# Performance work log

Hardware: AMD Instinct MI355X
Metric: run time of the kernel (lower is better)

Reference implementation:

```python
import jax, jax.numpy as jnp
import numpy as np

DIM, BIN = 128, 16
LN_EPS = 1e-5


def setup_inputs() -> dict:
    key = jax.random.key(0)
    ks = jax.random.split(key, 16)
    B, Ld, Lc, O = 4096, 50, 50, 64
    D_VOCAB, C_VOCAB = 100000, 1000
    inp = {
        "discrete_index": jax.random.randint(ks[0], (B, Ld), 0, D_VOCAB, dtype=jnp.int32),
        "discrete_mask": jax.random.randint(ks[1], (B, Ld), 0, 2, dtype=jnp.int32),
        "continue_value": jax.random.normal(ks[2], (B, Lc), dtype=jnp.float32),
        "continue_index": jax.random.randint(ks[3], (B, Lc), 0, C_VOCAB, dtype=jnp.int32),
        "continue_mask": jax.random.randint(ks[4], (B, Lc), 0, 2, dtype=jnp.int32),
        # learned parameters (last row = padding idx, zeroed like torch padding_idx init semantics)
        "disc_emb": jax.random.normal(ks[5], (D_VOCAB + 1, DIM), dtype=jnp.float32).at[D_VOCAB].set(0.0),
        "v_emb": jax.random.normal(ks[6], (C_VOCAB + 1, BIN), dtype=jnp.float32).at[C_VOCAB].set(0.0),
        "b1_emb": jax.random.normal(ks[7], (C_VOCAB + 1, BIN), dtype=jnp.float32).at[C_VOCAB].set(0.0),
        "w_emb": jax.random.normal(ks[8], (C_VOCAB + 1, DIM * BIN), dtype=jnp.float32).at[C_VOCAB].set(0.0),
        "b2_emb": jax.random.normal(ks[9], (C_VOCAB + 1, DIM), dtype=jnp.float32).at[C_VOCAB].set(0.0),
        "ln_gamma": jnp.ones((BIN,), dtype=jnp.float32),
        "ln_beta": jnp.zeros((BIN,), dtype=jnp.float32),
        "transform_matrix": jax.random.normal(ks[10], (O, Ld + Lc), dtype=jnp.float32),
    }
    return inp


def reference(discrete_index, discrete_mask, continue_value, continue_index, continue_mask,
              disc_emb, v_emb, b1_emb, w_emb, b2_emb, ln_gamma, ln_beta, transform_matrix):
    B, Lc = continue_index.shape
    # embedding gathers
    discrete_part = disc_emb[discrete_index]            # [B, Ld, D]
    v = v_emb[continue_index]                           # [B, Lc, BIN]
    b1 = b1_emb[continue_index]                         # [B, Lc, BIN]
    w = w_emb[continue_index].reshape(B, Lc, BIN, DIM)  # [B, Lc, BIN, D]
    b2 = b2_emb[continue_index]                         # [B, Lc, D]
    # per-token mini-MLP: LayerNorm(bin) + ReLU + bmm with per-token weight
    h = continue_value[..., None] * v + b1              # [B, Lc, BIN]
    mu = jnp.mean(h, axis=-1, keepdims=True)
    var = jnp.mean((h - mu) ** 2, axis=-1, keepdims=True)
    hn = (h - mu) * jax.lax.rsqrt(var + LN_EPS) * ln_gamma + ln_beta
    a = jax.nn.relu(hn)
    continuous_part = jnp.einsum('blk,blkd->bld', a, w) + b2  # [B, Lc, D]
    parts = jnp.concatenate([discrete_part, continuous_part], axis=1)  # [B, L, D]
    out = jnp.einsum('ol,bld->bod', transform_matrix, parts)           # [B, O, D]
    # mask (no-grad path in original)
    mvec = jnp.concatenate([1 - discrete_mask, 1 - continue_mask], axis=1).astype(jnp.float32)  # [B, L]
    full_mask = (1.0 - jnp.sign(jnp.einsum('ol,bl->bo', transform_matrix, mvec))).astype(jnp.int32)  # [B, O]
    return out, full_mask
```

## Files before the change

### kernel.cpp

```cpp
#include <hip/hip_runtime.h>
#include <hip/hip_bf16.h>

#define NB 4096
#define LD_ 50
#define LC_ 50
#define LTOT 100
#define DIM 128
#define BIN 16
#define NO 64
#define KPAD 128
#define LP 136
#define LN_EPS 1e-5f

#define DISC_ELEMS 12800128
#define DISC_VEC8  1600016
#define DISC_BLKS  6251
#define W_VEC8     256256
#define W_BLKS     1001
#define T_BLKS     32
#define CONV_BLKS  (DISC_BLKS + W_BLKS + T_BLKS)

typedef __attribute__((ext_vector_type(8))) short bf16x8;
typedef __attribute__((ext_vector_type(4))) float f32x4;

__device__ __forceinline__ unsigned f2bf(float f) {
    return (unsigned)__builtin_bit_cast(unsigned short, __float2bfloat16(f));
}
__device__ __forceinline__ float bf2f(unsigned u16) {
    return __builtin_bit_cast(float, u16 << 16);
}

__global__ __launch_bounds__(256) void conv_all(const float* __restrict__ disc,
                                                const float* __restrict__ w,
                                                const float* __restrict__ T,
                                                unsigned short* __restrict__ disc_bf,
                                                unsigned short* __restrict__ w_bf,
                                                unsigned short* __restrict__ Tbf) {
    const int bb = blockIdx.x;
    if (bb < DISC_BLKS) {
        size_t v = (size_t)bb * 256 + threadIdx.x;
        if (v < DISC_VEC8) {
            const float4* src = reinterpret_cast<const float4*>(disc + v * 8);
            float4 a = src[0], c = src[1];
            uint4 o;
            o.x = f2bf(a.x) | (f2bf(a.y) << 16);
            o.y = f2bf(a.z) | (f2bf(a.w) << 16);
            o.z = f2bf(c.x) | (f2bf(c.y) << 16);
            o.w = f2bf(c.z) | (f2bf(c.w) << 16);
            *reinterpret_cast<uint4*>(disc_bf + v * 8) = o;
        }
    } else if (bb < DISC_BLKS + W_BLKS) {
        size_t v = (size_t)(bb - DISC_BLKS) * 256 + threadIdx.x;
        const float4* src = reinterpret_cast<const float4*>(w + v * 8);
        float4 a = src[0], c = src[1];
        uint4 o;
        o.x = f2bf(a.x) | (f2bf(a.y) << 16);
        o.y = f2bf(a.z) | (f2bf(a.w) << 16);
        o.z = f2bf(c.x) | (f2bf(c.y) << 16);
        o.w = f2bf(c.z) | (f2bf(c.w) << 16);
        *reinterpret_cast<uint4*>(w_bf + v * 8) = o;
    } else {
        int t = (bb - DISC_BLKS - W_BLKS) * 256 + threadIdx.x;
        int o = t >> 7, k = t & 127;
        float v = (k < LTOT) ? T[o * LTOT + k] : 0.f;
        Tbf[t] = (unsigned short)f2bf(v);
    }
}

__global__ __launch_bounds__(512, 6) void fused_embed_kernel(
    const int* __restrict__ dindex,
    const int* __restrict__ dmask,
    const float* __restrict__ cval,
    const int* __restrict__ cindex,
    const int* __restrict__ cmask,
    const unsigned short* __restrict__ disc_bf,
    const float* __restrict__ v_emb,
    const float* __restrict__ b1_emb,
    const unsigned short* __restrict__ w_bf,
    const float* __restrict__ b2_emb,
    const float* __restrict__ ln_gamma,
    const float* __restrict__ ln_beta,
    const float* __restrict__ T,
    const unsigned short* __restrict__ Tbf,
    float* __restrict__ out,
    float* __restrict__ outmask)
{
    __shared__ unsigned short PbfT[DIM * LP];
    __shared__ float buf32[8][2][DIM];
    __shared__ float mvec[LTOT];

    const int b    = blockIdx.x;
    const int tid  = threadIdx.x;
    const int wave = tid >> 6;
    const int lane = tid & 63;
    const int d    = tid & 127;
    const int hh   = tid >> 7;

    if (tid < LTOT) {
        int m = (tid < LD_) ? dmask[b * LD_ + tid] : cmask[b * LC_ + (tid - LD_)];
        mvec[tid] = 1.0f - (float)m;
    }

    {
        unsigned short* row = &PbfT[d * LP];
        if (hh < 3) {
            *reinterpret_cast<uint2*>(&row[100 + hh * 8])     = make_uint2(0u, 0u);
            *reinterpret_cast<uint2*>(&row[100 + hh * 8 + 4]) = make_uint2(0u, 0u);
        } else {
            *reinterpret_cast<uint2*>(&row[124]) = make_uint2(0u, 0u);
        }
    }

    {
        int idxs[12];
        #pragma unroll
        for (int i = 0; i < 3; ++i) {
            const int l0 = (hh + 4 * i) * 4;
            #pragma unroll
            for (int j = 0; j < 4; ++j)
                idxs[i * 4 + j] = dindex[b * LD_ + l0 + j];
        }
        int it0 = 0, it1 = 0;
        if (hh == 0) { it0 = dindex[b * LD_ + 48]; it1 = dindex[b * LD_ + 49]; }

        unsigned short u[12];
        #pragma unroll
        for (int i = 0; i < 12; ++i)
            u[i] = disc_bf[(size_t)idxs[i] * DIM + d];
        unsigned short ut0 = 0, ut1 = 0;
        if (hh == 0) {
            ut0 = disc_bf[(size_t)it0 * DIM + d];
            ut1 = disc_bf[(size_t)it1 * DIM + d];
        }

        #pragma unroll
        for (int i = 0; i < 3; ++i) {
            const int l0 = (hh + 4 * i) * 4;
            unsigned lo = (unsigned)u[i*4+0] | ((unsigned)u[i*4+1] << 16);
            unsigned hi = (unsigned)u[i*4+2] | ((unsigned)u[i*4+3] << 16);
            *reinterpret_cast<uint2*>(&PbfT[d * LP + l0]) = make_uint2(lo, hi);
        }
        if (hh == 0) {
            *reinterpret_cast<unsigned int*>(&PbfT[d * LP + 48]) =
                (unsigned)ut0 | ((unsigned)ut1 << 16);
        }
    }

    {
        const int th    = lane >> 5;
        const int q     = lane & 31;
        const int bcast = lane & 32;

        int   ci[4];
        float cv[4];
        #pragma unroll
        for (int j = 0; j < 4; ++j) {
            const int p = wave + 8 * j;
            if (p < 25) {
                const int t = p * 2 + th;
                ci[j] = cindex[b * LC_ + t];
                cv[j] = cval[b * LC_ + t];
            }
        }

        #pragma unroll
        for (int j = 0; j < 4; ++j) {
            const int p = wave + 8 * j;
            if (p >= 25) break;
            const int   c  = ci[j];
            const float v0 = cv[j];

            float a_val = 0.f;
            if (q < 16) {
                float h = v0 * v_emb[c * BIN + q] + b1_emb[c * BIN + q];
                float s = h;
                s += __shfl_xor(s, 1, 16);
                s += __shfl_xor(s, 2, 16);
                s += __shfl_xor(s, 4, 16);
                s += __shfl_xor(s, 8, 16);
                float mu = s * (1.f / BIN);
                float e  = h - mu;
                float v2 = e * e;
                v2 += __shfl_xor(v2, 1, 16);
                v2 += __shfl_xor(v2, 2, 16);
                v2 += __shfl_xor(v2, 4, 16);
                v2 += __shfl_xor(v2, 8, 16);
                float rstd = rsqrtf(v2 * (1.f / BIN) + LN_EPS);
                a_val = fmaxf(e * rstd * ln_gamma[q] + ln_beta[q], 0.f);
            }

            float4 acc = *reinterpret_cast<const float4*>(b2_emb + (size_t)c * DIM + q * 4);
            const uint2* wp = reinterpret_cast<const uint2*>(w_bf + (size_t)c * (BIN * DIM) + q * 4);
            #pragma unroll
            for (int k = 0; k < BIN; ++k) {
                float ak = __shfl(a_val, bcast + k);
                uint2 wv = wp[k * 32];
                acc.x += ak * bf2f(wv.x & 0xffffu);
                acc.y += ak * bf2f(wv.x >> 16);
                acc.z += ak * bf2f(wv.y & 0xffffu);
                acc.w += ak * bf2f(wv.y >> 16);
            }

            *reinterpret_cast<float4*>(&buf32[wave][th][q * 4]) = acc;
            __builtin_amdgcn_wave_barrier();
            float x0 = buf32[wave][0][lane];
            float x1 = buf32[wave][1][lane];
            float x2 = buf32[wave][0][lane + 64];
            float x3 = buf32[wave][1][lane + 64];
            __builtin_amdgcn_wave_barrier();
            const int l0 = 50 + p * 2;
            *reinterpret_cast<unsigned int*>(&PbfT[lane * LP + l0]) =
                f2bf(x0) | (f2bf(x1) << 16);
            *reinterpret_cast<unsigned int*>(&PbfT[(lane + 64) * LP + l0]) =
                f2bf(x2) | (f2bf(x3) << 16);
        }
    }

    __syncthreads();

    if (tid < NO) {
        float s = 0.f;
        for (int l = 0; l < LTOT; ++l) s += T[tid * LTOT + l] * mvec[l];
        float sg = (s > 0.f) ? 1.f : ((s < 0.f) ? -1.f : 0.f);
        outmask[(size_t)b * NO + tid] = 1.f - sg;
    }

    {
        const int ot  = wave >> 1;
        const int nh  = wave & 1;
        const int r16 = lane & 15;
        const int g4  = lane >> 4;

        f32x4 acc[4];
        #pragma unroll
        for (int nt = 0; nt < 4; ++nt) acc[nt] = (f32x4){0.f, 0.f, 0.f, 0.f};

        bf16x8 afr[4];
        const unsigned short* Ta = Tbf + (16 * ot + r16) * KPAD + g4 * 8;
        #pragma unroll
        for (int kc = 0; kc < 4; ++kc)
            afr[kc] = *reinterpret_cast<const bf16x8*>(Ta + kc * 32);

        #pragma unroll
        for (int nt = 0; nt < 4; ++nt) {
            const unsigned short* Bp = &PbfT[((nh * 4 + nt) * 16 + r16) * LP + g4 * 8];
            #pragma unroll
            for (int kc = 0; kc < 4; ++kc) {
                bf16x8 bfr = *reinterpret_cast<const bf16x8*>(Bp + kc * 32);
                acc[nt] = __builtin_amdgcn_mfma_f32_16x16x32_bf16(afr[kc], bfr, acc[nt], 0, 0, 0);
            }
        }

        float* ob = out + (size_t)b * NO * DIM + (size_t)(16 * ot) * DIM + nh * 64;
        #pragma unroll
        for (int nt = 0; nt < 4; ++nt) {
            #pragma unroll
            for (int r = 0; r < 4; ++r) {
                ob[(g4 * 4 + r) * DIM + nt * 16 + r16] = acc[nt][r];
            }
        }
    }
}

extern "C" void kernel_launch(void* const* d_in, const int* in_sizes, int n_in,
                              void* d_out, int out_size, void* d_ws, size_t ws_size,
                              hipStream_t stream) {
    const int*   dindex  = (const int*)  d_in[0];
    const int*   dmask   = (const int*)  d_in[1];
    const float* cval    = (const float*)d_in[2];
    const int*   cindex  = (const int*)  d_in[3];
    const int*   cmask   = (const int*)  d_in[4];
    const float* disc_emb= (const float*)d_in[5];
    const float* v_emb   = (const float*)d_in[6];
    const float* b1_emb  = (const float*)d_in[7];
    const float* w_emb   = (const float*)d_in[8];
    const float* b2_emb  = (const float*)d_in[9];
    const float* lng     = (const float*)d_in[10];
    const float* lnb     = (const float*)d_in[11];
    const float* T       = (const float*)d_in[12];

    float* out     = (float*)d_out;
    float* outmask = out + (size_t)NB * NO * DIM;

    unsigned short* disc_bf = (unsigned short*)d_ws;
    unsigned short* w_bf    = (unsigned short*)((char*)d_ws + 25600256);
    unsigned short* Tbf     = (unsigned short*)((char*)d_ws + 25600256 + 4100096);

    hipLaunchKernelGGL(conv_all, dim3(CONV_BLKS), dim3(256), 0, stream,
                       disc_emb, w_emb, T, disc_bf, w_bf, Tbf);
    hipLaunchKernelGGL(fused_embed_kernel, dim3(NB), dim3(512), 0, stream,
                       dindex, dmask, cval, cindex, cmask,
                       disc_bf, v_emb, b1_emb, w_bf, b2_emb,
                       lng, lnb, T, Tbf, out, outmask);
}
```

Before: 322.4 us.

## Hoist all gathers before compute and use nontemporal loads/stores

Restructures the fused kernel so every global gather is issued up front: discrete-embedding indices, continuous indices and values, the v/b1/b2 rows and all 16 bf16 W rows per pair. The LayerNorm and per-token matvec run only after all loads are in flight, which is meant to overlap gather latency. The conversion kernel now uses nontemporal loads, and the output and mask stores are nontemporal to avoid polluting cache. Holding up to 64 uint2 W values per thread raises register pressure, which could cut occupancy under the 512x6 launch bound or cause spills.

```diff
diff --git a/kernel.cpp b/kernel.cpp
--- a/kernel.cpp
+++ b/kernel.cpp
@@ -12,16 +12,15 @@
 #define LP 136
 #define LN_EPS 1e-5f
 
-#define DISC_ELEMS 12800128
 #define DISC_VEC8  1600016
 #define DISC_BLKS  6251
-#define W_VEC8     256256
 #define W_BLKS     1001
 #define T_BLKS     32
 #define CONV_BLKS  (DISC_BLKS + W_BLKS + T_BLKS)
 
 typedef __attribute__((ext_vector_type(8))) short bf16x8;
 typedef __attribute__((ext_vector_type(4))) float f32x4;
+typedef __attribute__((ext_vector_type(4))) unsigned ui32x4;
 
 __device__ __forceinline__ unsigned f2bf(float f) {
     return (unsigned)__builtin_bit_cast(unsigned short, __float2bfloat16(f));
@@ -40,25 +39,27 @@
     if (bb < DISC_BLKS) {
         size_t v = (size_t)bb * 256 + threadIdx.x;
         if (v < DISC_VEC8) {
-            const float4* src = reinterpret_cast<const float4*>(disc + v * 8);
-            float4 a = src[0], c = src[1];
-            uint4 o;
-            o.x = f2bf(a.x) | (f2bf(a.y) << 16);
-            o.y = f2bf(a.z) | (f2bf(a.w) << 16);
-            o.z = f2bf(c.x) | (f2bf(c.y) << 16);
-            o.w = f2bf(c.z) | (f2bf(c.w) << 16);
-            *reinterpret_cast<uint4*>(disc_bf + v * 8) = o;
+            const f32x4* src = reinterpret_cast<const f32x4*>(disc + v * 8);
+            f32x4 a = __builtin_nontemporal_load(src);
+            f32x4 c = __builtin_nontemporal_load(src + 1);
+            ui32x4 o;
+            o[0] = f2bf(a[0]) | (f2bf(a[1]) << 16);
+            o[1] = f2bf(a[2]) | (f2bf(a[3]) << 16);
+            o[2] = f2bf(c[0]) | (f2bf(c[1]) << 16);
+            o[3] = f2bf(c[2]) | (f2bf(c[3]) << 16);
+            *reinterpret_cast<ui32x4*>(disc_bf + v * 8) = o;
         }
     } else if (bb < DISC_BLKS + W_BLKS) {
         size_t v = (size_t)(bb - DISC_BLKS) * 256 + threadIdx.x;
-        const float4* src = reinterpret_cast<const float4*>(w + v * 8);
-        float4 a = src[0], c = src[1];
-        uint4 o;
-        o.x = f2bf(a.x) | (f2bf(a.y) << 16);
-        o.y = f2bf(a.z) | (f2bf(a.w) << 16);
-        o.z = f2bf(c.x) | (f2bf(c.y) << 16);
-        o.w = f2bf(c.z) | (f2bf(c.w) << 16);
-        *reinterpret_cast<uint4*>(w_bf + v * 8) = o;
+        const f32x4* src = reinterpret_cast<const f32x4*>(w + v * 8);
+        f32x4 a = __builtin_nontemporal_load(src);
+        f32x4 c = __builtin_nontemporal_load(src + 1);
+        ui32x4 o;
+        o[0] = f2bf(a[0]) | (f2bf(a[1]) << 16);
+        o[1] = f2bf(a[2]) | (f2bf(a[3]) << 16);
+        o[2] = f2bf(c[0]) | (f2bf(c[1]) << 16);
+        o[3] = f2bf(c[2]) | (f2bf(c[3]) << 16);
+        *reinterpret_cast<ui32x4*>(w_bf + v * 8) = o;
     } else {
         int t = (bb - DISC_BLKS - W_BLKS) * 256 + threadIdx.x;
         int o = t >> 7, k = t & 127;
@@ -111,109 +112,120 @@
         }
     }
 
-    {
-        int idxs[12];
-        #pragma unroll
-        for (int i = 0; i < 3; ++i) {
-            const int l0 = (hh + 4 * i) * 4;
-            #pragma unroll
-            for (int j = 0; j < 4; ++j)
-                idxs[i * 4 + j] = dindex[b * LD_ + l0 + j];
-        }
-        int it0 = 0, it1 = 0;
-        if (hh == 0) { it0 = dindex[b * LD_ + 48]; it1 = dindex[b * LD_ + 49]; }
-
-        unsigned short u[12];
-        #pragma unroll
-        for (int i = 0; i < 12; ++i)
-            u[i] = disc_bf[(size_t)idxs[i] * DIM + d];
-        unsigned short ut0 = 0, ut1 = 0;
-        if (hh == 0) {
-            ut0 = disc_bf[(size_t)it0 * DIM + d];
-            ut1 = disc_bf[(size_t)it1 * DIM + d];
-        }
-
-        #pragma unroll
-        for (int i = 0; i < 3; ++i) {
-            const int l0 = (hh + 4 * i) * 4;
-            unsigned lo = (unsigned)u[i*4+0] | ((unsigned)u[i*4+1] << 16);
-            unsigned hi = (unsigned)u[i*4+2] | ((unsigned)u[i*4+3] << 16);
-            *reinterpret_cast<uint2*>(&PbfT[d * LP + l0]) = make_uint2(lo, hi);
-        }
-        if (hh == 0) {
-            *reinterpret_cast<unsigned int*>(&PbfT[d * LP + 48]) =
-                (unsigned)ut0 | ((unsigned)ut1 << 16);
-        }
-    }
-
-    {
-        const int th    = lane >> 5;
-        const int q     = lane & 31;
-        const int bcast = lane & 32;
-
-        int   ci[4];
-        float cv[4];
-        #pragma unroll
-        for (int j = 0; j < 4; ++j) {
+    int idxs[12];
+    #pragma unroll
+    for (int i = 0; i < 3; ++i) {
+        const int l0 = (hh + 4 * i) * 4;
+        #pragma unroll
+        for (int j = 0; j < 4; ++j)
+            idxs[i * 4 + j] = dindex[b * LD_ + l0 + j];
+    }
+    int it0 = 0, it1 = 0;
+    if (hh == 0) { it0 = dindex[b * LD_ + 48]; it1 = dindex[b * LD_ + 49]; }
+
+    const int th    = lane >> 5;
+    const int q     = lane & 31;
+    const int bcast = lane & 32;
+    const int npair = (wave == 0) ? 4 : 3;
+
+    int   ci[4]; float cv[4];
+    #pragma unroll
+    for (int j = 0; j < 4; ++j) {
+        if (j < npair) {
             const int p = wave + 8 * j;
-            if (p < 25) {
-                const int t = p * 2 + th;
-                ci[j] = cindex[b * LC_ + t];
-                cv[j] = cval[b * LC_ + t];
+            const int t = p * 2 + th;
+            ci[j] = cindex[b * LC_ + t];
+            cv[j] = cval[b * LC_ + t];
+        }
+    }
+
+    unsigned short u[12];
+    #pragma unroll
+    for (int i = 0; i < 12; ++i)
+        u[i] = disc_bf[(size_t)idxs[i] * DIM + d];
+    unsigned short ut0 = 0, ut1 = 0;
+    if (hh == 0) {
+        ut0 = disc_bf[(size_t)it0 * DIM + d];
+        ut1 = disc_bf[(size_t)it1 * DIM + d];
+    }
+
+    float ve[4], b1e[4];
+    float4 b2r[4];
+    uint2  wr[4][16];
+    #pragma unroll
+    for (int j = 0; j < 4; ++j) {
+        if (j < npair) {
+            const int c = ci[j];
+            if (q < 16) {
+                ve[j]  = v_emb[c * BIN + q];
+                b1e[j] = b1_emb[c * BIN + q];
             }
-        }
-
-        #pragma unroll
-        for (int j = 0; j < 4; ++j) {
-            const int p = wave + 8 * j;
-            if (p >= 25) break;
-            const int   c  = ci[j];
-            const float v0 = cv[j];
-
-            float a_val = 0.f;
-            if (q < 16) {
-                float h = v0 * v_emb[c * BIN + q] + b1_emb[c * BIN + q];
-                float s = h;
-                s += __shfl_xor(s, 1, 16);
-                s += __shfl_xor(s, 2, 16);
-                s += __shfl_xor(s, 4, 16);
-                s += __shfl_xor(s, 8, 16);
-                float mu = s * (1.f / BIN);
-                float e  = h - mu;
-                float v2 = e * e;
-                v2 += __shfl_xor(v2, 1, 16);
-                v2 += __shfl_xor(v2, 2, 16);
-                v2 += __shfl_xor(v2, 4, 16);
-                v2 += __shfl_xor(v2, 8, 16);
-                float rstd = rsqrtf(v2 * (1.f / BIN) + LN_EPS);
-                a_val = fmaxf(e * rstd * ln_gamma[q] + ln_beta[q], 0.f);
-            }
-
-            float4 acc = *reinterpret_cast<const float4*>(b2_emb + (size_t)c * DIM + q * 4);
+            b2r[j] = *reinterpret_cast<const float4*>(b2_emb + (size_t)c * DIM + q * 4);
             const uint2* wp = reinterpret_cast<const uint2*>(w_bf + (size_t)c * (BIN * DIM) + q * 4);
             #pragma unroll
-            for (int k = 0; k < BIN; ++k) {
-                float ak = __shfl(a_val, bcast + k);
-                uint2 wv = wp[k * 32];
-                acc.x += ak * bf2f(wv.x & 0xffffu);
-                acc.y += ak * bf2f(wv.x >> 16);
-                acc.z += ak * bf2f(wv.y & 0xffffu);
-                acc.w += ak * bf2f(wv.y >> 16);
-            }
-
-            *reinterpret_cast<float4*>(&buf32[wave][th][q * 4]) = acc;
-            __builtin_amdgcn_wave_barrier();
-            float x0 = buf32[wave][0][lane];
-            float x1 = buf32[wave][1][lane];
-            float x2 = buf32[wave][0][lane + 64];
-            float x3 = buf32[wave][1][lane + 64];
-            __builtin_amdgcn_wave_barrier();
-            const int l0 = 50 + p * 2;
-            *reinterpret_cast<unsigned int*>(&PbfT[lane * LP + l0]) =
-                f2bf(x0) | (f2bf(x1) << 16);
-            *reinterpret_cast<unsigned int*>(&PbfT[(lane + 64) * LP + l0]) =
-                f2bf(x2) | (f2bf(x3) << 16);
-        }
+            for (int k = 0; k < BIN; ++k) wr[j][k] = wp[k * 32];
+        }
+    }
+
+    #pragma unroll
+    for (int i = 0; i < 3; ++i) {
+        const int l0 = (hh + 4 * i) * 4;
+        unsigned lo = (unsigned)u[i*4+0] | ((unsigned)u[i*4+1] << 16);
+        unsigned hi = (unsigned)u[i*4+2] | ((unsigned)u[i*4+3] << 16);
+        *reinterpret_cast<uint2*>(&PbfT[d * LP + l0]) = make_uint2(lo, hi);
+    }
+    if (hh == 0) {
+        *reinterpret_cast<unsigned int*>(&PbfT[d * LP + 48]) =
+            (unsigned)ut0 | ((unsigned)ut1 << 16);
+    }
+
+    #pragma unroll
+    for (int j = 0; j < 4; ++j) {
+        if (j >= npair) break;
+        const int p = wave + 8 * j;
+
+        float a_val = 0.f;
+        if (q < 16) {
+            float h = cv[j] * ve[j] + b1e[j];
+            float s = h;
+            s += __shfl_xor(s, 1, 16);
+            s += __shfl_xor(s, 2, 16);
+            s += __shfl_xor(s, 4, 16);
+            s += __shfl_xor(s, 8, 16);
+            float mu = s * (1.f / BIN);
+            float e  = h - mu;
+            float v2 = e * e;
+            v2 += __shfl_xor(v2, 1, 16);
+            v2 += __shfl_xor(v2, 2, 16);
+            v2 += __shfl_xor(v2, 4, 16);
+            v2 += __shfl_xor(v2, 8, 16);
+            float rstd = rsqrtf(v2 * (1.f / BIN) + LN_EPS);
+            a_val = fmaxf(e * rstd * ln_gamma[q] + ln_beta[q], 0.f);
+        }
+
+        float4 acc = b2r[j];
+        #pragma unroll
+        for (int k = 0; k < BIN; ++k) {
+            float ak = __shfl(a_val, bcast + k);
+            uint2 wv = wr[j][k];
+            acc.x += ak * bf2f(wv.x & 0xffffu);
+            acc.y += ak * bf2f(wv.x >> 16);
+            acc.z += ak * bf2f(wv.y & 0xffffu);
+            acc.w += ak * bf2f(wv.y >> 16);
+        }
+
+        *reinterpret_cast<float4*>(&buf32[wave][th][q * 4]) = acc;
+        __builtin_amdgcn_wave_barrier();
+        float x0 = buf32[wave][0][lane];
+        float x1 = buf32[wave][1][lane];
+        float x2 = buf32[wave][0][lane + 64];
+        float x3 = buf32[wave][1][lane + 64];
+        __builtin_amdgcn_wave_barrier();
+        const int l0 = 50 + p * 2;
+        *reinterpret_cast<unsigned int*>(&PbfT[lane * LP + l0]) =
+            f2bf(x0) | (f2bf(x1) << 16);
+        *reinterpret_cast<unsigned int*>(&PbfT[(lane + 64) * LP + l0]) =
+            f2bf(x2) | (f2bf(x3) << 16);
     }
 
     __syncthreads();
@@ -222,7 +234,7 @@
         float s = 0.f;
         for (int l = 0; l < LTOT; ++l) s += T[tid * LTOT + l] * mvec[l];
         float sg = (s > 0.f) ? 1.f : ((s < 0.f) ? -1.f : 0.f);
-        outmask[(size_t)b * NO + tid] = 1.f - sg;
+        __builtin_nontemporal_store(1.f - sg, &outmask[(size_t)b * NO + tid]);
     }
 
     {
@@ -256,7 +268,8 @@
         for (int nt = 0; nt < 4; ++nt) {
             #pragma unroll
             for (int r = 0; r < 4; ++r) {
-                ob[(g4 * 4 + r) * DIM + nt * 16 + r16] = acc[nt][r];
+                __builtin_nontemporal_store(acc[nt][r],
+                    &ob[(g4 * 4 + r) * DIM + nt * 16 + r16]);
             }
         }
     }
```

Measured after the change: 538.4 us. 67.0% more time.
